# Optimization experiments

Measured on AMD Instinct MI355X. Metric: run time of the kernel, lower is better.

Reference implementation:

```python
import jax, jax.numpy as jnp
import numpy as np

BLOCK = 128  # block_size for the blockwise Hadamard rotation

def hadamard_matrix(n: int) -> np.ndarray:
    """Normalized Sylvester Hadamard matrix H_n / sqrt(n) (n must be a power of 2)."""
    H = np.array([[1.0]], dtype=np.float32)
    while H.shape[0] < n:
        H = np.block([[H, H], [H, -H]])
    return (H / np.sqrt(np.float32(n))).astype(np.float32)

def setup_inputs() -> dict:
    key = jax.random.key(0)
    k1, k2, k3 = jax.random.split(key, 3)
    B, S, D, O = 2, 4096, 4096, 4096
    x = jax.random.normal(k1, (B, S, D), dtype=jnp.float32)
    W = jax.random.normal(k2, (O, D), dtype=jnp.float32) * 0.02  # nn.Linear weight [out, in]
    b = jax.random.normal(k3, (O,), dtype=jnp.float32) * 0.02
    return {"x": x, "W": W, "b": b}

def reference(x, W, b):
    n = x.shape[-1]
    H = jnp.asarray(hadamard_matrix(BLOCK))  # [BLOCK, BLOCK], includes 1/sqrt(BLOCK)
    # blockwise normalized Hadamard on last dim: view as [..., n//BLOCK, BLOCK]
    y = x.reshape(*x.shape[:-1], n // BLOCK, BLOCK)
    y = jnp.einsum('...kb,bc->...kc', y, H)
    y = y.reshape(x.shape)
    # linear projection: y @ W^T + b
    return jnp.einsum('bsd,od->bso', y, W) + b
```

## Files before the change

### kernel.cpp

```cpp
#include <hip/hip_runtime.h>
#include <hip/hip_bf16.h>
#include <stdint.h>

#define AS1 __attribute__((address_space(1)))
#define AS3 __attribute__((address_space(3)))

typedef __attribute__((ext_vector_type(8))) short short8;
typedef __attribute__((ext_vector_type(4))) float f32x4;
typedef __attribute__((ext_vector_type(4))) int i32x4;

__device__ __forceinline__ unsigned short f2bf(float f) {
  return __builtin_bit_cast(unsigned short, __float2bfloat16(f));
}

__global__ __launch_bounds__(256) void quant_prep(const float* __restrict__ W,
                                                  signed char* __restrict__ Wq,
                                                  float* __restrict__ sw,
                                                  const float* __restrict__ x,
                                                  signed char* __restrict__ Xq,
                                                  float* __restrict__ sx,
                                                  int wrows, int Kd) {
  __shared__ float red[4];
  const int bid = blockIdx.x;
  const int tid = threadIdx.x;
  const bool isW = bid < wrows;
  const int row = isW ? bid : bid - wrows;
  const float* src = (isW ? W : x) + (size_t)row * Kd + tid * 16;

  float v[16];
  {
    float4 f0 = ((const float4*)src)[0];
    float4 f1 = ((const float4*)src)[1];
    float4 f2 = ((const float4*)src)[2];
    float4 f3 = ((const float4*)src)[3];
    v[0] = f0.x; v[1] = f0.y; v[2] = f0.z; v[3] = f0.w;
    v[4] = f1.x; v[5] = f1.y; v[6] = f1.z; v[7] = f1.w;
    v[8] = f2.x; v[9] = f2.y; v[10] = f2.z; v[11] = f2.w;
    v[12] = f3.x; v[13] = f3.y; v[14] = f3.z; v[15] = f3.w;
  }

  if (isW) {
#pragma unroll
    for (int m = 1; m <= 8; m <<= 1) {
#pragma unroll
      for (int j = 0; j < 16; ++j) {
        if ((j & m) == 0) {
          float lo = v[j], hi = v[j + m];
          v[j] = lo + hi;
          v[j + m] = lo - hi;
        }
      }
    }
    const int g = tid & 7;
#pragma unroll
    for (int m = 1; m <= 4; m <<= 1) {
#pragma unroll
      for (int j = 0; j < 16; ++j) {
        float p = __shfl_xor(v[j], m, 64);
        v[j] = (g & m) ? (p - v[j]) : (v[j] + p);
      }
    }
    const float s = 0.08838834764831845f;
#pragma unroll
    for (int j = 0; j < 16; ++j) v[j] *= s;
  }

  float am = 0.f;
#pragma unroll
  for (int j = 0; j < 16; ++j) am = fmaxf(am, fabsf(v[j]));
#pragma unroll
  for (int m = 1; m < 64; m <<= 1) am = fmaxf(am, __shfl_xor(am, m, 64));
  if ((tid & 63) == 0) red[tid >> 6] = am;
  __syncthreads();
  am = fmaxf(fmaxf(red[0], red[1]), fmaxf(red[2], red[3]));

  const float inv = (am > 1e-30f) ? (127.0f / am) : 0.f;
  union { uint4 u; signed char c[16]; } pk;
#pragma unroll
  for (int j = 0; j < 16; ++j) {
    float q = __builtin_rintf(v[j] * inv);
    q = fminf(127.f, fmaxf(-127.f, q));
    pk.c[j] = (signed char)(int)q;
  }
  signed char* dst = (isW ? Wq : Xq) + (size_t)row * Kd + tid * 16;
  *(uint4*)dst = pk.u;
  if (tid == 0) (isW ? sw : sx)[row] = am / 127.0f;
}

__device__ __forceinline__ void gload16(const void* g, void* l) {
  __builtin_amdgcn_global_load_lds((const AS1 unsigned int*)g,
                                   (AS3 unsigned int*)l, 16, 0, 0);
}

#define BM 256
#define BN 256
#define PL(base_, mat_, kh_) ((base_) + (((mat_) * 2 + (kh_)) * 16384))

__global__ __launch_bounds__(512, 2) void gemm256_i8(const signed char* __restrict__ Xq,
                                                     const signed char* __restrict__ Wq,
                                                     const float* __restrict__ sx,
                                                     const float* __restrict__ sw,
                                                     const float* __restrict__ bias,
                                                     float* __restrict__ out,
                                                     int M, int N, int K) {
  __shared__ __align__(16) char lds[131072];

  const int tid = threadIdx.x;
  const int lane = tid & 63;
  const int wid = tid >> 6;
  const int wm = wid >> 2;
  const int wn = wid & 3;

  const int nwg = gridDim.x;
  const int cpx = nwg >> 3;
  const int swz = (blockIdx.x & 7) * cpx + (blockIdx.x >> 3);
  const int nbn = N / BN;
  const int m0 = (swz / nbn) * BM;
  const int n0 = (swz % nbn) * BN;

  const size_t Kb = (size_t)K;

  const int dphys0 = tid * 16;
  const int dphys1 = tid * 16 + 8192;
  const char* srcA[2][2];
  const char* srcB[2][2];
  {
    const int dv[2] = {dphys0, dphys1};
#pragma unroll
    for (int rd = 0; rd < 2; ++rd) {
      const int d = dv[rd];
      const int l = d ^ (((d >> 7) & 3) << 4);
      const int row = l >> 6;
      const int cb = l & 63;
#pragma unroll
      for (int kh = 0; kh < 2; ++kh) {
        srcA[kh][rd] = (const char*)Xq + (size_t)(m0 + row) * Kb + kh * 64 + cb;
        srcB[kh][rd] = (const char*)Wq + (size_t)(n0 + row) * Kb + kh * 64 + cb;
      }
    }
  }

  const int q = lane >> 4;
  const int fr = lane & 15;
  int oA[2][4], oB[4];
#pragma unroll
  for (int mh = 0; mh < 2; ++mh)
#pragma unroll
    for (int mi = 0; mi < 4; ++mi) {
      int row = wm * 128 + mh * 64 + mi * 16 + fr;
      int byt = row * 64 + q * 16;
      oA[mh][mi] = byt ^ (((byt >> 7) & 3) << 4);
    }
#pragma unroll
  for (int ni = 0; ni < 4; ++ni) {
    int row = wn * 64 + ni * 16 + fr;
    int byt = row * 64 + q * 16;
    oB[ni] = byt ^ (((byt >> 7) & 3) << 4);
  }

  i32x4 acc[8][4];
#pragma unroll
  for (int i = 0; i < 8; ++i)
#pragma unroll
    for (int j = 0; j < 4; ++j) acc[i][j] = (i32x4){0, 0, 0, 0};

  const int NT = K / 128;
  char* const lb0 = lds;
  char* const lb1 = lds + 65536;

#define STAGE(mat_, kh_, base_, toff_)                                       \
  do {                                                                       \
    const char* s0_ = ((mat_) ? srcB : srcA)[kh_][0] + (toff_);              \
    const char* s1_ = ((mat_) ? srcB : srcA)[kh_][1] + (toff_);              \
    gload16(s0_, PL(base_, mat_, kh_) + dphys0);                             \
    gload16(s1_, PL(base_, mat_, kh_) + dphys1);                             \
  } while (0)

#define READ_A4(dst_, base_, kh_, mh_)                                       \
  do {                                                                       \
    const char* p_ = PL(base_, 0, kh_);                                      \
    _Pragma("unroll") for (int mi = 0; mi < 4; ++mi)                         \
        dst_[mi] = *(const i32x4*)(p_ + oA[mh_][mi]);                        \
  } while (0)

#define READ_B4(dst_, base_, kh_)                                            \
  do {                                                                       \
    const char* p_ = PL(base_, 1, kh_);                                      \
    _Pragma("unroll") for (int ni = 0; ni < 4; ++ni)                         \
        dst_[ni] = *(const i32x4*)(p_ + oB[ni]);                             \
  } while (0)

#define MFMA16(mh_, a_, b_)                                                  \
  do {                                                                       \
    __builtin_amdgcn_s_setprio(1);                                           \
    _Pragma("unroll") for (int mi = 0; mi < 4; ++mi)                         \
        _Pragma("unroll") for (int ni = 0; ni < 4; ++ni)                     \
            acc[(mh_)*4 + mi][ni] = __builtin_amdgcn_mfma_i32_16x16x64_i8(   \
                a_[mi], b_[ni], acc[(mh_)*4 + mi][ni], 0, 0, 0);             \
    __builtin_amdgcn_s_setprio(0);                                           \
    __builtin_amdgcn_sched_barrier(0);                                       \
  } while (0)

#define LGKM(n_)                                                             \
  asm volatile("s_waitcnt lgkmcnt(" #n_ ")" ::: "memory");                   \
  __builtin_amdgcn_sched_barrier(0)

  gload16(srcA[0][0], PL(lb0, 0, 0) + dphys0);
  gload16(srcA[0][1], PL(lb0, 0, 0) + dphys1);
  gload16(srcB[0][0], PL(lb0, 1, 0) + dphys0);
  gload16(srcB[0][1], PL(lb0, 1, 0) + dphys1);
  gload16(srcA[1][0], PL(lb0, 0, 1) + dphys0);
  gload16(srcA[1][1], PL(lb0, 0, 1) + dphys1);
  gload16(srcB[1][0], PL(lb0, 1, 1) + dphys0);
  gload16(srcB[1][1], PL(lb0, 1, 1) + dphys1);
  gload16(srcA[0][0] + 128, PL(lb1, 0, 0) + dphys0);
  gload16(srcA[0][1] + 128, PL(lb1, 0, 0) + dphys1);
  gload16(srcB[0][0] + 128, PL(lb1, 1, 0) + dphys0);
  gload16(srcB[0][1] + 128, PL(lb1, 1, 0) + dphys1);
  asm volatile("s_waitcnt vmcnt(4)" ::: "memory");
  __builtin_amdgcn_s_barrier();
  asm volatile("" ::: "memory");

  i32x4 av0[4], av1[4], bv0[4], bv1[4];
  READ_A4(av0, lb0, 0, 0);
  READ_B4(bv0, lb0, 0);

  for (int t = 0; t < NT; ++t) {
    char* const cb = (t & 1) ? lb1 : lb0;
    char* const db = (t & 1) ? lb0 : lb1;
    int tn1 = t + 1; if (tn1 >= NT) tn1 -= NT;
    int tn2 = t + 2; if (tn2 >= NT) tn2 -= NT;
    const size_t toff1 = (size_t)tn1 * 128;
    const size_t toff2 = (size_t)tn2 * 128;

    __builtin_amdgcn_s_barrier();
    asm volatile("" ::: "memory");
    READ_A4(av1, cb, 0, 1);
    STAGE(0, 1, db, toff1);
    LGKM(4);
    MFMA16(0, av0, bv0);

    asm volatile("s_waitcnt vmcnt(6)" ::: "memory");
    __builtin_amdgcn_s_barrier();
    asm volatile("" ::: "memory");
    READ_A4(av0, cb, 1, 0);
    READ_B4(bv1, cb, 1);
    STAGE(1, 1, db, toff1);
    LGKM(8);
    MFMA16(1, av1, bv0);

    __builtin_amdgcn_s_barrier();
    asm volatile("" ::: "memory");
    READ_A4(av1, cb, 1, 1);
    STAGE(0, 0, cb, toff2);
    LGKM(4);
    MFMA16(0, av0, bv1);

    asm volatile("s_waitcnt vmcnt(6)" ::: "memory");
    __builtin_amdgcn_s_barrier();
    asm volatile("" ::: "memory");
    READ_A4(av0, db, 0, 0);
    READ_B4(bv0, db, 0);
    STAGE(1, 0, cb, toff2);
    LGKM(8);
    MFMA16(1, av1, bv1);
  }
  asm volatile("s_waitcnt vmcnt(0)" ::: "memory");

  const int orow = m0 + wm * 128;
  const int ocol = n0 + wn * 64;
  const int rsub = q << 2;
#pragma unroll
  for (int ni = 0; ni < 4; ++ni) {
    const int col = ocol + ni * 16 + fr;
    const float swc = sw[col];
    const float bc = bias[col];
#pragma unroll
    for (int am = 0; am < 8; ++am) {
      const int rbase = orow + (am >> 2) * 64 + (am & 3) * 16 + rsub;
#pragma unroll
      for (int r = 0; r < 4; ++r) {
        const int row = rbase + r;
        out[(size_t)row * N + col] =
            (float)acc[am][ni][r] * (sx[row] * swc) + bc;
      }
    }
  }
}

__global__ __launch_bounds__(256) void fwht_only(const float* __restrict__ W,
                                                 unsigned short* __restrict__ Wp,
                                                 int total_vec) {
  int t = blockIdx.x * blockDim.x + threadIdx.x;
  if (t >= total_vec) return;
  float4 r0 = ((const float4*)W)[2 * t];
  float4 r1 = ((const float4*)W)[2 * t + 1];
  float v[8] = {r0.x, r0.y, r0.z, r0.w, r1.x, r1.y, r1.z, r1.w};
#pragma unroll
  for (int m = 1; m <= 4; m <<= 1) {
#pragma unroll
    for (int j = 0; j < 8; ++j) {
      if ((j & m) == 0) {
        float lo = v[j], hi = v[j + m];
        v[j] = lo + hi;
        v[j + m] = lo - hi;
      }
    }
  }
  const int g = t & 15;
#pragma unroll
  for (int m = 1; m <= 8; m <<= 1) {
#pragma unroll
    for (int j = 0; j < 8; ++j) {
      float p = __shfl_xor(v[j], m, 64);
      v[j] = (g & m) ? (p - v[j]) : (v[j] + p);
    }
  }
  const float s = 0.08838834764831845f;
  uint4 outv;
  unsigned short* ou = (unsigned short*)&outv;
#pragma unroll
  for (int j = 0; j < 8; ++j) ou[j] = f2bf(v[j] * s);
  ((uint4*)Wp)[t] = outv;
}

__global__ __launch_bounds__(256) void gemm128_a32(const float* __restrict__ X,
                                                   const unsigned short* __restrict__ Wp,
                                                   const float* __restrict__ bias,
                                                   float* __restrict__ out,
                                                   int M, int N, int K) {
  __shared__ __align__(16) unsigned short lA[128 * 32];
  __shared__ __align__(16) unsigned short lB[128 * 32];
  const int tid = threadIdx.x;
  const int lane = tid & 63;
  const int wid = tid >> 6;
  const int wr = wid >> 1, wc = wid & 1;
  const int nbn = N / 128;
  const int bm = blockIdx.x / nbn, bn = blockIdx.x % nbn;
  const int m0 = bm * 128, n0 = bn * 128;
  f32x4 acc[4][4];
#pragma unroll
  for (int i = 0; i < 4; ++i)
#pragma unroll
    for (int j = 0; j < 4; ++j) acc[i][j] = (f32x4){0.f, 0.f, 0.f, 0.f};
  const size_t Kb = (size_t)K * 2;
  const int off0 = tid * 16, off1 = off0 + 4096;
  const int r0 = off0 >> 6, c0 = off0 & 63;
  const int r1 = off1 >> 6, c1 = off1 & 63;
  const char* Bg0 = (const char*)Wp + (size_t)(n0 + r0) * Kb + c0;
  const char* Bg1 = (const char*)Wp + (size_t)(n0 + r1) * Kb + c1;
  char* lB0 = (char*)lB + off0;
  char* lB1 = (char*)lB + off1;
  const int arow = tid >> 1;
  const int acol = (tid & 1) * 16;
  const float* Af = X + (size_t)(m0 + arow) * K + acol;
  unsigned short* lAw = &lA[arow * 32 + acol];
  const int fr = lane & 15;
  const int kc = (lane >> 4) << 3;
  const unsigned short* pA = &lA[(wr * 64 + fr) * 32 + kc];
  const unsigned short* pB = &lB[(wc * 64 + fr) * 32 + kc];
  for (int k0 = 0; k0 < K; k0 += 32) {
    const int kb = k0 << 1;
    gload16(Bg0 + kb, lB0);
    gload16(Bg1 + kb, lB1);
    const float* src = Af + k0;
    float4 f0 = *(const float4*)(src + 0);
    float4 f1 = *(const float4*)(src + 4);
    float4 f2 = *(const float4*)(src + 8);
    float4 f3 = *(const float4*)(src + 12);
    union { uint4 u[2]; unsigned short s[16]; } pk;
    float vv[16] = {f0.x, f0.y, f0.z, f0.w, f1.x, f1.y, f1.z, f1.w,
                    f2.x, f2.y, f2.z, f2.w, f3.x, f3.y, f3.z, f3.w};
#pragma unroll
    for (int j = 0; j < 16; ++j) pk.s[j] = f2bf(vv[j]);
    ((uint4*)lAw)[0] = pk.u[0];
    ((uint4*)(lAw + 8))[0] = pk.u[1];
    __syncthreads();
    short8 af[4], bfr[4];
#pragma unroll
    for (int mi = 0; mi < 4; ++mi) af[mi] = *(const short8*)(pA + mi * 16 * 32);
#pragma unroll
    for (int ni = 0; ni < 4; ++ni) bfr[ni] = *(const short8*)(pB + ni * 16 * 32);
#pragma unroll
    for (int mi = 0; mi < 4; ++mi)
#pragma unroll
      for (int ni = 0; ni < 4; ++ni)
        acc[mi][ni] = __builtin_amdgcn_mfma_f32_16x16x32_bf16(af[mi], bfr[ni],
                                                              acc[mi][ni], 0, 0, 0);
    __syncthreads();
  }
  const int orow0 = m0 + wr * 64;
  const int ocol0 = n0 + wc * 64;
  const int rsub = (lane >> 4) << 2;
#pragma unroll
  for (int ni = 0; ni < 4; ++ni) {
    const int col = ocol0 + ni * 16 + fr;
    const float bc = bias[col];
#pragma unroll
    for (int mi = 0; mi < 4; ++mi)
#pragma unroll
      for (int r = 0; r < 4; ++r)
        out[(size_t)(orow0 + mi * 16 + rsub + r) * N + col] = acc[mi][ni][r] + bc;
  }
}

extern "C" void kernel_launch(void* const* d_in, const int* in_sizes, int n_in,
                              void* d_out, int out_size, void* d_ws, size_t ws_size,
                              hipStream_t stream) {
  const float* x = (const float*)d_in[0];
  const float* W = (const float*)d_in[1];
  const float* b = (const float*)d_in[2];
  float* out = (float*)d_out;

  const int O = in_sizes[2];
  const int K = in_sizes[1] / O;
  const int M = in_sizes[0] / K;

  const size_t wqB = (size_t)O * K;
  const size_t xqB = (size_t)M * K;
  const size_t need = wqB + xqB + (size_t)(O + M) * 4 + 256;

  if (ws_size >= need) {
    signed char* Wq = (signed char*)d_ws;
    signed char* Xq = (signed char*)d_ws + wqB;
    float* sw = (float*)((char*)d_ws + wqB + xqB);
    float* sx = sw + O;
    quant_prep<<<O + M, 256, 0, stream>>>(W, Wq, sw, x, Xq, sx, O, K);
    dim3 grid((M / BM) * (O / BN));
    gemm256_i8<<<grid, 512, 0, stream>>>(Xq, Wq, sx, sw, b, out, M, O, K);
  } else {
    unsigned short* Wp = (unsigned short*)d_ws;
    const int wvec = (O * K) / 8;
    fwht_only<<<(wvec + 255) / 256, 256, 0, stream>>>(W, Wp, wvec);
    dim3 grid((M / 128) * (O / 128));
    gemm128_a32<<<grid, 256, 0, stream>>>(x, Wp, b, out, M, O, K);
  }
}
```

Measured before the change: 194.4 us.

## Replace 256x256 int8 GEMM with 128x256 tile, triple-buffered K=64 pipeline

Replaces the 256x256 int8 GEMM kernel with a 128x256 tile that steps K in chunks of 64. It uses a three-slot LDS ring buffer in place of two 64 KB buffers and a simpler single-phase loop. The smaller LDS footprint and accumulator set aim to fit more blocks per CU and improve latency hiding. In exchange, each tile reuses data less, which raises global/L2 traffic, and there is one barrier per 64-wide K step.

```diff
diff --git a/kernel.cpp b/kernel.cpp
--- a/kernel.cpp
+++ b/kernel.cpp
@@ -92,18 +92,18 @@
                                    (AS3 unsigned int*)l, 16, 0, 0);
 }
 
-#define BM 256
-#define BN 256
-#define PL(base_, mat_, kh_) ((base_) + (((mat_) * 2 + (kh_)) * 16384))
-
-__global__ __launch_bounds__(512, 2) void gemm256_i8(const signed char* __restrict__ Xq,
-                                                     const signed char* __restrict__ Wq,
-                                                     const float* __restrict__ sx,
-                                                     const float* __restrict__ sw,
-                                                     const float* __restrict__ bias,
-                                                     float* __restrict__ out,
-                                                     int M, int N, int K) {
-  __shared__ __align__(16) char lds[131072];
+#define BM2 128
+#define BN2 256
+#define SLOTSZ 24576
+
+__global__ __launch_bounds__(512, 4) void gemm_i8_2blk(const signed char* __restrict__ Xq,
+                                                       const signed char* __restrict__ Wq,
+                                                       const float* __restrict__ sx,
+                                                       const float* __restrict__ sw,
+                                                       const float* __restrict__ bias,
+                                                       float* __restrict__ out,
+                                                       int M, int N, int K) {
+  __shared__ __align__(16) char lds[3 * SLOTSZ];
 
   const int tid = threadIdx.x;
   const int lane = tid & 63;
@@ -113,161 +113,97 @@
 
   const int nwg = gridDim.x;
   const int cpx = nwg >> 3;
-  const int swz = (blockIdx.x & 7) * cpx + (blockIdx.x >> 3);
-  const int nbn = N / BN;
-  const int m0 = (swz / nbn) * BM;
-  const int n0 = (swz % nbn) * BN;
-
+  const int swzb = (blockIdx.x & 7) * cpx + (blockIdx.x >> 3);
+  const int nbn = N / BN2;
+  const int m0 = (swzb / nbn) * BM2;
+  const int n0 = (swzb % nbn) * BN2;
   const size_t Kb = (size_t)K;
 
-  const int dphys0 = tid * 16;
-  const int dphys1 = tid * 16 + 8192;
-  const char* srcA[2][2];
-  const char* srcB[2][2];
+  const int dA = tid * 16;
+  const int dB0 = tid * 16;
+  const int dB1 = tid * 16 + 8192;
+  const char* srcA;
+  const char* srcB0;
+  const char* srcB1;
   {
-    const int dv[2] = {dphys0, dphys1};
-#pragma unroll
-    for (int rd = 0; rd < 2; ++rd) {
-      const int d = dv[rd];
-      const int l = d ^ (((d >> 7) & 3) << 4);
-      const int row = l >> 6;
-      const int cb = l & 63;
-#pragma unroll
-      for (int kh = 0; kh < 2; ++kh) {
-        srcA[kh][rd] = (const char*)Xq + (size_t)(m0 + row) * Kb + kh * 64 + cb;
-        srcB[kh][rd] = (const char*)Wq + (size_t)(n0 + row) * Kb + kh * 64 + cb;
-      }
-    }
+    int l = dA ^ (((dA >> 7) & 3) << 4);
+    srcA = (const char*)Xq + (size_t)(m0 + (l >> 6)) * Kb + (l & 63);
+    l = dB0 ^ (((dB0 >> 7) & 3) << 4);
+    srcB0 = (const char*)Wq + (size_t)(n0 + (l >> 6)) * Kb + (l & 63);
+    l = dB1 ^ (((dB1 >> 7) & 3) << 4);
+    srcB1 = (const char*)Wq + (size_t)(n0 + (l >> 6)) * Kb + (l & 63);
   }
 
   const int q = lane >> 4;
   const int fr = lane & 15;
-  int oA[2][4], oB[4];
-#pragma unroll
-  for (int mh = 0; mh < 2; ++mh)
-#pragma unroll
-    for (int mi = 0; mi < 4; ++mi) {
-      int row = wm * 128 + mh * 64 + mi * 16 + fr;
-      int byt = row * 64 + q * 16;
-      oA[mh][mi] = byt ^ (((byt >> 7) & 3) << 4);
-    }
+  int oA[4], oB[4];
+#pragma unroll
+  for (int mi = 0; mi < 4; ++mi) {
+    int row = wm * 64 + mi * 16 + fr;
+    int byt = row * 64 + q * 16;
+    oA[mi] = byt ^ (((byt >> 7) & 3) << 4);
+  }
 #pragma unroll
   for (int ni = 0; ni < 4; ++ni) {
     int row = wn * 64 + ni * 16 + fr;
     int byt = row * 64 + q * 16;
-    oB[ni] = byt ^ (((byt >> 7) & 3) << 4);
-  }
-
-  i32x4 acc[8][4];
-#pragma unroll
-  for (int i = 0; i < 8; ++i)
+    oB[ni] = 8192 + (byt ^ (((byt >> 7) & 3) << 4));
+  }
+
+  i32x4 acc[4][4];
+#pragma unroll
+  for (int i = 0; i < 4; ++i)
 #pragma unroll
     for (int j = 0; j < 4; ++j) acc[i][j] = (i32x4){0, 0, 0, 0};
 
-  const int NT = K / 128;
-  char* const lb0 = lds;
-  char* const lb1 = lds + 65536;
-
-#define STAGE(mat_, kh_, base_, toff_)                                       \
+#define STAGE3(sl_, ko_)                                                     \
   do {                                                                       \
-    const char* s0_ = ((mat_) ? srcB : srcA)[kh_][0] + (toff_);              \
-    const char* s1_ = ((mat_) ? srcB : srcA)[kh_][1] + (toff_);              \
-    gload16(s0_, PL(base_, mat_, kh_) + dphys0);                             \
-    gload16(s1_, PL(base_, mat_, kh_) + dphys1);                             \
+    gload16(srcA + (ko_), (sl_) + dA);                                       \
+    gload16(srcB0 + (ko_), (sl_) + 8192 + dB0);                              \
+    gload16(srcB1 + (ko_), (sl_) + 8192 + dB1);                              \
   } while (0)
 
-#define READ_A4(dst_, base_, kh_, mh_)                                       \
-  do {                                                                       \
-    const char* p_ = PL(base_, 0, kh_);                                      \
-    _Pragma("unroll") for (int mi = 0; mi < 4; ++mi)                         \
-        dst_[mi] = *(const i32x4*)(p_ + oA[mh_][mi]);                        \
-  } while (0)
-
-#define READ_B4(dst_, base_, kh_)                                            \
-  do {                                                                       \
-    const char* p_ = PL(base_, 1, kh_);                                      \
-    _Pragma("unroll") for (int ni = 0; ni < 4; ++ni)                         \
-        dst_[ni] = *(const i32x4*)(p_ + oB[ni]);                             \
-  } while (0)
-
-#define MFMA16(mh_, a_, b_)                                                  \
-  do {                                                                       \
-    __builtin_amdgcn_s_setprio(1);                                           \
-    _Pragma("unroll") for (int mi = 0; mi < 4; ++mi)                         \
-        _Pragma("unroll") for (int ni = 0; ni < 4; ++ni)                     \
-            acc[(mh_)*4 + mi][ni] = __builtin_amdgcn_mfma_i32_16x16x64_i8(   \
-                a_[mi], b_[ni], acc[(mh_)*4 + mi][ni], 0, 0, 0);             \
-    __builtin_amdgcn_s_setprio(0);                                           \
-    __builtin_amdgcn_sched_barrier(0);                                       \
-  } while (0)
-
-#define LGKM(n_)                                                             \
-  asm volatile("s_waitcnt lgkmcnt(" #n_ ")" ::: "memory");                   \
-  __builtin_amdgcn_sched_barrier(0)
-
-  gload16(srcA[0][0], PL(lb0, 0, 0) + dphys0);
-  gload16(srcA[0][1], PL(lb0, 0, 0) + dphys1);
-  gload16(srcB[0][0], PL(lb0, 1, 0) + dphys0);
-  gload16(srcB[0][1], PL(lb0, 1, 0) + dphys1);
-  gload16(srcA[1][0], PL(lb0, 0, 1) + dphys0);
-  gload16(srcA[1][1], PL(lb0, 0, 1) + dphys1);
-  gload16(srcB[1][0], PL(lb0, 1, 1) + dphys0);
-  gload16(srcB[1][1], PL(lb0, 1, 1) + dphys1);
-  gload16(srcA[0][0] + 128, PL(lb1, 0, 0) + dphys0);
-  gload16(srcA[0][1] + 128, PL(lb1, 0, 0) + dphys1);
-  gload16(srcB[0][0] + 128, PL(lb1, 1, 0) + dphys0);
-  gload16(srcB[0][1] + 128, PL(lb1, 1, 0) + dphys1);
-  asm volatile("s_waitcnt vmcnt(4)" ::: "memory");
+  STAGE3(lds, 0);
+  STAGE3(lds + SLOTSZ, 64);
+  asm volatile("s_waitcnt vmcnt(3)" ::: "memory");
   __builtin_amdgcn_s_barrier();
   asm volatile("" ::: "memory");
 
-  i32x4 av0[4], av1[4], bv0[4], bv1[4];
-  READ_A4(av0, lb0, 0, 0);
-  READ_B4(bv0, lb0, 0);
+  char* s0 = lds;
+  char* s1 = lds + SLOTSZ;
+  char* s2 = lds + 2 * SLOTSZ;
+  int koff = 128;
+  const int NT = K >> 6;
 
   for (int t = 0; t < NT; ++t) {
-    char* const cb = (t & 1) ? lb1 : lb0;
-    char* const db = (t & 1) ? lb0 : lb1;
-    int tn1 = t + 1; if (tn1 >= NT) tn1 -= NT;
-    int tn2 = t + 2; if (tn2 >= NT) tn2 -= NT;
-    const size_t toff1 = (size_t)tn1 * 128;
-    const size_t toff2 = (size_t)tn2 * 128;
-
+    i32x4 av[4], bv[4];
+#pragma unroll
+    for (int mi = 0; mi < 4; ++mi) av[mi] = *(const i32x4*)(s0 + oA[mi]);
+#pragma unroll
+    for (int ni = 0; ni < 4; ++ni) bv[ni] = *(const i32x4*)(s0 + oB[ni]);
+    STAGE3(s2, koff);
+    koff += 64;
+    if (koff >= K) koff -= K;
+    asm volatile("s_waitcnt lgkmcnt(0)" ::: "memory");
+    __builtin_amdgcn_sched_barrier(0);
+    __builtin_amdgcn_s_setprio(1);
+#pragma unroll
+    for (int mi = 0; mi < 4; ++mi)
+#pragma unroll
+      for (int ni = 0; ni < 4; ++ni)
+        acc[mi][ni] = __builtin_amdgcn_mfma_i32_16x16x64_i8(av[mi], bv[ni],
+                                                            acc[mi][ni], 0, 0, 0);
+    __builtin_amdgcn_s_setprio(0);
+    __builtin_amdgcn_sched_barrier(0);
+
+    char* tp = s0; s0 = s1; s1 = s2; s2 = tp;
+    asm volatile("s_waitcnt vmcnt(3)" ::: "memory");
     __builtin_amdgcn_s_barrier();
     asm volatile("" ::: "memory");
-    READ_A4(av1, cb, 0, 1);
-    STAGE(0, 1, db, toff1);
-    LGKM(4);
-    MFMA16(0, av0, bv0);
-
-    asm volatile("s_waitcnt vmcnt(6)" ::: "memory");
-    __builtin_amdgcn_s_barrier();
-    asm volatile("" ::: "memory");
-    READ_A4(av0, cb, 1, 0);
-    READ_B4(bv1, cb, 1);
-    STAGE(1, 1, db, toff1);
-    LGKM(8);
-    MFMA16(1, av1, bv0);
-
-    __builtin_amdgcn_s_barrier();
-    asm volatile("" ::: "memory");
-    READ_A4(av1, cb, 1, 1);
-    STAGE(0, 0, cb, toff2);
-    LGKM(4);
-    MFMA16(0, av0, bv1);
-
-    asm volatile("s_waitcnt vmcnt(6)" ::: "memory");
-    __builtin_amdgcn_s_barrier();
-    asm volatile("" ::: "memory");
-    READ_A4(av0, db, 0, 0);
-    READ_B4(bv0, db, 0);
-    STAGE(1, 0, cb, toff2);
-    LGKM(8);
-    MFMA16(1, av1, bv1);
   }
   asm volatile("s_waitcnt vmcnt(0)" ::: "memory");
 
-  const int orow = m0 + wm * 128;
+  const int orow = m0 + wm * 64;
   const int ocol = n0 + wn * 64;
   const int rsub = q << 2;
 #pragma unroll
@@ -276,16 +212,17 @@
     const float swc = sw[col];
     const float bc = bias[col];
 #pragma unroll
-    for (int am = 0; am < 8; ++am) {
-      const int rbase = orow + (am >> 2) * 64 + (am & 3) * 16 + rsub;
+    for (int mi = 0; mi < 4; ++mi) {
+      const int rbase = orow + mi * 16 + rsub;
 #pragma unroll
       for (int r = 0; r < 4; ++r) {
         const int row = rbase + r;
         out[(size_t)row * N + col] =
-            (float)acc[am][ni][r] * (sx[row] * swc) + bc;
+            (float)acc[mi][ni][r] * (sx[row] * swc) + bc;
       }
     }
   }
+#undef STAGE3
 }
 
 __global__ __launch_bounds__(256) void fwht_only(const float* __restrict__ W,
@@ -426,8 +363,8 @@
     float* sw = (float*)((char*)d_ws + wqB + xqB);
     float* sx = sw + O;
     quant_prep<<<O + M, 256, 0, stream>>>(W, Wq, sw, x, Xq, sx, O, K);
-    dim3 grid((M / BM) * (O / BN));
-    gemm256_i8<<<grid, 512, 0, stream>>>(Xq, Wq, sx, sw, b, out, M, O, K);
+    dim3 grid((M / BM2) * (O / BN2));
+    gemm_i8_2blk<<<grid, 512, 0, stream>>>(Xq, Wq, sx, sw, b, out, M, O, K);
   } else {
     unsigned short* Wp = (unsigned short*)d_ws;
     const int wvec = (O * K) / 8;
```

After: 206.8 us. 6.4% more time.
